# Performance work log

Measured on AMD Instinct MI355X. Metric: run time of the kernel, lower is better.

Reference implementation:

```python
import jax, jax.numpy as jnp
import numpy as np

EPS_MSG = 1e-7   # GENConv message epsilon
BN_EPS = 1e-5    # BatchNorm1d eps
NUM_GRAPHS = 1024


def _linear(x, W, b):
    return x @ W + b


def _batchnorm(x, gamma, beta):
    # training-mode batch statistics over the node dimension
    mu = jnp.mean(x, axis=0)
    var = jnp.mean((x - mu) ** 2, axis=0)
    return (x - mu) * jax.lax.rsqrt(var + BN_EPS) * gamma + beta


def _genconv(x, src, dst, e, t, W1, b1, gamma, beta, W2, b2, num_nodes):
    # message: relu(x_j + edge_attr) + eps, shape [E, H]
    msg = jax.nn.relu(x[src] + e) + EPS_MSG
    # learnable softmax aggregation over each destination's neighborhood
    s = msg * t
    m = jax.lax.stop_gradient(jax.ops.segment_max(s, dst, num_segments=num_nodes))
    m = jnp.where(jnp.isfinite(m), m, 0.0)
    ex = jnp.exp(s - m[dst])
    denom = jax.ops.segment_sum(ex, dst, num_segments=num_nodes)
    alpha = ex / (denom[dst] + 1e-16)
    agg = jax.ops.segment_sum(msg * alpha, dst, num_segments=num_nodes)  # [N, H]
    # GENConv MLP([H, 2H, H], norm='batch') applied to x + aggregated messages
    h = x + agg
    h = _linear(h, W1, b1)
    h = _batchnorm(h, gamma, beta)
    h = jax.nn.relu(h)
    return _linear(h, W2, b2)


def setup_inputs() -> dict:
    key = jax.random.key(0)
    N, E, FIN, FE, H, L, G, OUT = 50000, 1000000, 32, 16, 64, 4, NUM_GRAPHS, 1
    ks = jax.random.split(key, 32)

    def rn(k, shape, fan_in):
        return jax.random.normal(k, shape, dtype=jnp.float32) * (1.0 / np.sqrt(fan_in))

    inp = {}
    inp["x"] = jax.random.normal(ks[0], (N, FIN), dtype=jnp.float32)
    inp["edge_attr"] = jax.random.normal(ks[1], (E, FE), dtype=jnp.float32)
    inp["edge_index"] = jax.random.randint(ks[2], (2, E), 0, N)
    inp["batch"] = jnp.sort(jax.random.randint(ks[3], (N,), 0, G))
    # atom encoder: Linear(FIN,H) ReLU Linear(H,H) ReLU
    inp["atom_W1"] = rn(ks[4], (FIN, H), FIN); inp["atom_b1"] = jnp.zeros((H,), jnp.float32)
    inp["atom_W2"] = rn(ks[5], (H, H), H);     inp["atom_b2"] = jnp.zeros((H,), jnp.float32)
    # bond encoder: Linear(FE,H) ReLU Linear(H,H) ReLU
    inp["bond_W1"] = rn(ks[6], (FE, H), FE);   inp["bond_b1"] = jnp.zeros((H,), jnp.float32)
    inp["bond_W2"] = rn(ks[7], (H, H), H);     inp["bond_b2"] = jnp.zeros((H,), jnp.float32)
    # stacked GENConv params (L layers)
    inp["conv_t"] = jnp.ones((L,), jnp.float32)
    inp["conv_W1"] = rn(ks[8], (L, H, 2 * H), H)
    inp["conv_b1"] = jnp.zeros((L, 2 * H), jnp.float32)
    inp["conv_gamma"] = jnp.ones((L, 2 * H), jnp.float32)
    inp["conv_beta"] = jnp.zeros((L, 2 * H), jnp.float32)
    inp["conv_W2"] = rn(ks[9], (L, 2 * H, H), 2 * H)
    inp["conv_b2"] = jnp.zeros((L, H), jnp.float32)
    # head
    inp["lin1_W"] = rn(ks[10], (H, H), H);     inp["lin1_b"] = jnp.zeros((H,), jnp.float32)
    inp["lin2_W"] = rn(ks[11], (H, OUT), H);   inp["lin2_b"] = jnp.zeros((OUT,), jnp.float32)
    return inp


def reference(x, edge_attr, atom_W1, atom_b1, atom_W2, atom_b2,
              bond_W1, bond_b1, bond_W2, bond_b2,
              conv_t, conv_W1, conv_b1, conv_gamma, conv_beta, conv_W2, conv_b2,
              lin1_W, lin1_b, lin2_W, lin2_b,
              edge_index, batch):
    N = x.shape[0]
    src, dst = edge_index[0], edge_index[1]
    h = jax.nn.relu(_linear(jax.nn.relu(_linear(x, atom_W1, atom_b1)), atom_W2, atom_b2))
    e = jax.nn.relu(_linear(jax.nn.relu(_linear(edge_attr, bond_W1, bond_b1)), bond_W2, bond_b2))
    L = conv_t.shape[0]
    for i in range(L):
        h = _genconv(h, src, dst, e, conv_t[i], conv_W1[i], conv_b1[i],
                     conv_gamma[i], conv_beta[i], conv_W2[i], conv_b2[i], N)
        if i < L - 1:
            h = jax.nn.relu(h)
    g = jax.ops.segment_sum(h, batch, num_segments=NUM_GRAPHS)  # global_add_pool
    g = jax.nn.relu(_linear(g, lin1_W, lin1_b))
    return _linear(g, lin2_W, lin2_b)
```

## Files before the change

kernel.cpp:

```cpp
#include <hip/hip_runtime.h>
#include <hip/hip_bf16.h>
#include <math.h>

typedef __attribute__((ext_vector_type(8))) short bf16x8;
typedef __attribute__((ext_vector_type(4))) float f32x4;

__device__ inline unsigned f2bf(float f) {
    union { __hip_bfloat16 h; unsigned short u; } cv;
    cv.h = __float2bfloat16(f);
    return (unsigned)cv.u;
}


__global__ void k_hist(const int* __restrict__ dst, int* __restrict__ counts, int E) {
    int e = blockIdx.x * blockDim.x + threadIdx.x;
    if (e < E) atomicAdd(&counts[dst[e]], 1);
}

__global__ void k_scan1(const int* __restrict__ counts, int* __restrict__ row_ptr,
                        int* __restrict__ csum, int n) {
    __shared__ int buf[1024];
    int tid = threadIdx.x;
    int base = blockIdx.x * 1024;
    int v = (base + tid < n) ? counts[base + tid] : 0;
    buf[tid] = v;
    __syncthreads();
    int inc = v;
    for (int off = 1; off < 1024; off <<= 1) {
        int add = (tid >= off) ? buf[tid - off] : 0;
        __syncthreads();
        inc += add;
        buf[tid] = inc;
        __syncthreads();
    }
    if (base + tid < n) row_ptr[base + tid] = inc - v;
    if (tid == 1023) csum[blockIdx.x] = inc;
}

__global__ void k_scan2(int* __restrict__ csum, int nc, int* __restrict__ total) {
    if (threadIdx.x == 0) {
        int run = 0;
        for (int i = 0; i < nc; ++i) { int c = csum[i]; csum[i] = run; run += c; }
        *total = run;
    }
}

__global__ void k_scan3(int* __restrict__ row_ptr, const int* __restrict__ csum,
                        const int* __restrict__ total, int n) {
    int i = blockIdx.x * blockDim.x + threadIdx.x;
    if (i < n) row_ptr[i] += csum[i >> 10];
    if (i == 0) row_ptr[n] = *total;
}

#define ECH 4096
__global__ __launch_bounds__(256) void k_scatter(const int* __restrict__ src,
                          const int* __restrict__ dst,
                          const int* __restrict__ row_ptr, int* __restrict__ fill,
                          int2* __restrict__ spe, int E, int NS) {
    int bs = blockIdx.x & 7;
    int chunk = blockIdx.x >> 3;
    int base = chunk * ECH;
    int lo = bs * NS, hi = lo + NS;
#pragma unroll 1
    for (int j = 0; j < ECH / 256; ++j) {
        int e = base + j * 256 + threadIdx.x;
        if (e < E) {
            int d = dst[e];
            if (d >= lo && d < hi) {
                int pos = row_ptr[d] + atomicAdd(&fill[d], 1);
                spe[pos] = make_int2(src[e], e);
            }
        }
    }
}

__global__ void k_gptr(const int* __restrict__ batch, int* __restrict__ gptr, int n, int G) {
    int i = blockIdx.x * blockDim.x + threadIdx.x;
    if (i > n) return;
    if (i == 0) {
        int b0 = batch[0];
        for (int g = 0; g <= b0; ++g) gptr[g] = 0;
    } else if (i == n) {
        int bl = batch[n - 1];
        for (int g = bl + 1; g <= G; ++g) gptr[g] = n;
    } else {
        int b = batch[i], pb = batch[i - 1];
        for (int g = pb + 1; g <= b; ++g) gptr[g] = i;
    }
}


__global__ void k_wt(const float* __restrict__ W1, const float* __restrict__ W2,
                     float* __restrict__ W1t, unsigned short* __restrict__ W2tb) {
    int tid = blockIdx.x * blockDim.x + threadIdx.x;
    if (tid < 1024) {
        int j = tid / 16, k = tid % 16;
        W1t[j * 16 + k] = W1[k * 64 + j];
    }
    if (tid < 4096) {
        int j = tid / 64, k = tid % 64;
        W2tb[j * 64 + k] = (unsigned short)f2bf(W2[k * 64 + j]);
    }
}


#define TM 128
__global__ __launch_bounds__(256) void k_atom(const float* __restrict__ x,
        const float* __restrict__ W1, const float* __restrict__ b1,
        const float* __restrict__ W2, const float* __restrict__ b2,
        float* __restrict__ out, int M) {
    __shared__ float sU[TM * 65];
    __shared__ float sW1[32 * 64];
    __shared__ float sW2[64 * 64];
    __shared__ float sB1[64], sB2[64];
#define A_IN(r, c) sU[(r) * 33 + (c)]
#define A_T1(r, c) sU[(r) * 65 + (c)]
    int tid = threadIdx.x;
    int base = blockIdx.x * TM;
    for (int i = tid; i < 32 * 64 / 4; i += 256) ((float4*)sW1)[i] = ((const float4*)W1)[i];
    for (int i = tid; i < 64 * 64 / 4; i += 256) ((float4*)sW2)[i] = ((const float4*)W2)[i];
    if (tid < 64) { sB1[tid] = b1[tid]; sB2[tid] = b2[tid]; }
    for (int i = tid; i < TM * 32 / 4; i += 256) {
        int r = i / 8, c4 = i % 8;
        int row = base + r;
        float4 v = (row < M) ? ((const float4*)(x + (long)row * 32))[c4] : make_float4(0, 0, 0, 0);
        A_IN(r, c4 * 4 + 0) = v.x; A_IN(r, c4 * 4 + 1) = v.y;
        A_IN(r, c4 * 4 + 2) = v.z; A_IN(r, c4 * 4 + 3) = v.w;
    }
    __syncthreads();
    int r0 = (tid / 16) * 8;
    int c0 = (tid % 16) * 4;
    float acc[8][4];
#pragma unroll
    for (int i = 0; i < 8; i++)
#pragma unroll
        for (int j = 0; j < 4; j++) acc[i][j] = sB1[c0 + j];
    for (int k = 0; k < 32; k++) {
        float a[8], b[4];
#pragma unroll
        for (int i = 0; i < 8; i++) a[i] = A_IN(r0 + i, k);
#pragma unroll
        for (int j = 0; j < 4; j++) b[j] = sW1[k * 64 + c0 + j];
#pragma unroll
        for (int i = 0; i < 8; i++)
#pragma unroll
            for (int j = 0; j < 4; j++) acc[i][j] += a[i] * b[j];
    }
    __syncthreads();
#pragma unroll
    for (int i = 0; i < 8; i++)
#pragma unroll
        for (int j = 0; j < 4; j++) A_T1(r0 + i, c0 + j) = fmaxf(acc[i][j], 0.f);
    __syncthreads();
#pragma unroll
    for (int i = 0; i < 8; i++)
#pragma unroll
        for (int j = 0; j < 4; j++) acc[i][j] = sB2[c0 + j];
    for (int k = 0; k < 64; k++) {
        float a[8], b[4];
#pragma unroll
        for (int i = 0; i < 8; i++) a[i] = A_T1(r0 + i, k);
#pragma unroll
        for (int j = 0; j < 4; j++) b[j] = sW2[k * 64 + c0 + j];
#pragma unroll
        for (int i = 0; i < 8; i++)
#pragma unroll
            for (int j = 0; j < 4; j++) acc[i][j] += a[i] * b[j];
    }
#pragma unroll
    for (int i = 0; i < 8; i++) {
        int row = base + r0 + i;
        if (row < M) {
            float4 v = make_float4(fmaxf(acc[i][0], 0.f), fmaxf(acc[i][1], 0.f),
                                   fmaxf(acc[i][2], 0.f), fmaxf(acc[i][3], 0.f));
            *(float4*)(out + (long)row * 64 + c0) = v;
        }
    }
}


__global__ __launch_bounds__(256) void k_bond(const float* __restrict__ ea,
        const int2* __restrict__ spe,
        const float* __restrict__ W1t, const float* __restrict__ b1,
        const unsigned short* __restrict__ W2tb, const float* __restrict__ b2,
        __hip_bfloat16* __restrict__ e_out, int E) {
    __shared__ unsigned sT1[128 * 32];
    __shared__ unsigned sW2[64 * 32];
    int tid = threadIdx.x;

    for (int i = tid; i < 2048; i += 256) {
        int rw = i >> 5, cp = i & 31;
        sW2[rw * 32 + (cp ^ ((rw & 7) << 2))] = ((const unsigned*)W2tb)[i];
    }

    int ed = tid & 127;
    int h0 = __builtin_amdgcn_readfirstlane(tid >> 7);
    long gid = (long)blockIdx.x * 128 + ed;
    float in[16];
    if (gid < (long)E) {
        int src_e = spe[gid].y;
        const float4* er = (const float4*)(ea + (long)src_e * 16);
        float4 q0 = er[0], q1 = er[1], q2 = er[2], q3 = er[3];
        in[0] = q0.x; in[1] = q0.y; in[2] = q0.z; in[3] = q0.w;
        in[4] = q1.x; in[5] = q1.y; in[6] = q1.z; in[7] = q1.w;
        in[8] = q2.x; in[9] = q2.y; in[10] = q2.z; in[11] = q2.w;
        in[12] = q3.x; in[13] = q3.y; in[14] = q3.z; in[15] = q3.w;
    } else {
#pragma unroll
        for (int k = 0; k < 16; ++k) in[k] = 0.f;
    }

#pragma unroll
    for (int c = 0; c < 16; ++c) {
        float a0 = b1[h0 * 32 + 2 * c];
        float a1 = b1[h0 * 32 + 2 * c + 1];
#pragma unroll
        for (int k = 0; k < 16; ++k) {
            a0 = fmaf(in[k], W1t[(h0 * 32 + 2 * c) * 16 + k], a0);
            a1 = fmaf(in[k], W1t[(h0 * 32 + 2 * c + 1) * 16 + k], a1);
        }
        unsigned v = f2bf(fmaxf(a0, 0.f)) | (f2bf(fmaxf(a1, 0.f)) << 16);
        int cp = h0 * 16 + c;
        sT1[ed * 32 + (cp ^ ((ed & 7) << 2))] = v;
    }
    __syncthreads();

    int wv = tid >> 6, lane = tid & 63;
    int lr = lane & 15, q = lane >> 4;
    bf16x8 bf[4][2];
#pragma unroll
    for (int nt = 0; nt < 4; ++nt)
#pragma unroll
        for (int ks = 0; ks < 2; ++ks) {
            int rw = nt * 16 + lr;
            int u = rw * 32 + ((ks * 16 + q * 4) ^ ((rw & 7) << 2));
            bf[nt][ks] = *(const bf16x8*)&sW2[u];
        }
    f32x4 acc[2][4];
#pragma unroll
    for (int mt = 0; mt < 2; ++mt)
#pragma unroll
        for (int nt = 0; nt < 4; ++nt) {
            float bias = b2[nt * 16 + lr];
            f32x4 c0; c0[0] = bias; c0[1] = bias; c0[2] = bias; c0[3] = bias;
            acc[mt][nt] = c0;
        }
#pragma unroll
    for (int mt = 0; mt < 2; ++mt) {
        int rw = (wv * 2 + mt) * 16 + lr;
#pragma unroll
        for (int ks = 0; ks < 2; ++ks) {
            int u = rw * 32 + ((ks * 16 + q * 4) ^ ((rw & 7) << 2));
            bf16x8 af = *(const bf16x8*)&sT1[u];
#pragma unroll
            for (int nt = 0; nt < 4; ++nt)
                acc[mt][nt] = __builtin_amdgcn_mfma_f32_16x16x32_bf16(
                    af, bf[nt][ks], acc[mt][nt], 0, 0, 0);
        }
    }
    unsigned short* ob = (unsigned short*)e_out;
#pragma unroll
    for (int mt = 0; mt < 2; ++mt)
#pragma unroll
        for (int nt = 0; nt < 4; ++nt)
#pragma unroll
            for (int i = 0; i < 4; ++i) {
                long row = (long)blockIdx.x * 128 + (wv * 2 + mt) * 16 + q * 4 + i;
                if (row < (long)E)
                    ob[row * 64 + nt * 16 + lr] =
                        (unsigned short)f2bf(fmaxf(acc[mt][nt][i], 0.f));
            }
}


__global__ __launch_bounds__(256) void k_agg(const float* __restrict__ h,
        const __hip_bfloat16* __restrict__ eperm, const int2* __restrict__ spe,
        const int* __restrict__ row_ptr, const float* __restrict__ t_ptr, int layer,
        float* __restrict__ y, int n) {
    int wid = blockIdx.x * 4 + (threadIdx.x >> 6);
    int lane = threadIdx.x & 63;
    if (wid >= n) return;
    wid = __builtin_amdgcn_readfirstlane(wid);
    float tval = t_ptr[layer];
    int beg = row_ptr[wid], end = row_ptr[wid + 1];
    float m = -INFINITY, den = 0.f, num = 0.f;
    int i = beg;
    int rem = (end - beg) & 3;
    for (int r = 0; r < rem; ++r, ++i) {
        int s = spe[i].x;
        float ev = __bfloat162float(eperm[(long)i * 64 + lane]);
        float hv = h[(long)s * 64 + lane];
        float msg = fmaxf(hv + ev, 0.f) + 1e-7f;
        float sv = msg * tval;
        float mn = fmaxf(m, sv);
        float sc = __expf(m - mn);
        float w = __expf(sv - mn);
        den = den * sc + w;
        num = num * sc + w * msg;
        m = mn;
    }
    for (; i < end; i += 4) {
        int s0 = spe[i].x, s1 = spe[i + 1].x, s2 = spe[i + 2].x, s3 = spe[i + 3].x;
        float ev0 = __bfloat162float(eperm[(long)i * 64 + lane]);
        float ev1 = __bfloat162float(eperm[(long)(i + 1) * 64 + lane]);
        float ev2 = __bfloat162float(eperm[(long)(i + 2) * 64 + lane]);
        float ev3 = __bfloat162float(eperm[(long)(i + 3) * 64 + lane]);
        float hv0 = h[(long)s0 * 64 + lane];
        float hv1 = h[(long)s1 * 64 + lane];
        float hv2 = h[(long)s2 * 64 + lane];
        float hv3 = h[(long)s3 * 64 + lane];
        float msg0 = fmaxf(hv0 + ev0, 0.f) + 1e-7f;
        float msg1 = fmaxf(hv1 + ev1, 0.f) + 1e-7f;
        float msg2 = fmaxf(hv2 + ev2, 0.f) + 1e-7f;
        float msg3 = fmaxf(hv3 + ev3, 0.f) + 1e-7f;
        float sv0 = msg0 * tval, sv1 = msg1 * tval;
        float sv2 = msg2 * tval, sv3 = msg3 * tval;
        float mn = fmaxf(fmaxf(fmaxf(m, sv0), fmaxf(sv1, sv2)), sv3);
        float sc = __expf(m - mn);
        float w0 = __expf(sv0 - mn);
        float w1 = __expf(sv1 - mn);
        float w2 = __expf(sv2 - mn);
        float w3 = __expf(sv3 - mn);
        den = den * sc + ((w0 + w1) + (w2 + w3));
        num = num * sc + ((w0 * msg0 + w1 * msg1) + (w2 * msg2 + w3 * msg3));
        m = mn;
    }
    float agg = (end > beg) ? num / (den + 1e-16f) : 0.f;
    y[(long)wid * 64 + lane] = h[(long)wid * 64 + lane] + agg;
}


__global__ __launch_bounds__(256) void k_gemm1(const float* __restrict__ y,
        const float* __restrict__ W1, const float* __restrict__ b1,
        float* __restrict__ h1, float* __restrict__ part, int n) {
    __shared__ float sA[64][65];
    __shared__ float sW[64 * 128];
    __shared__ float sB[128];
    __shared__ float sS[8][128];
    __shared__ float sS2[8][128];
    int tid = threadIdx.x;
    int base = blockIdx.x * 64;
    for (int i = tid; i < 64 * 128 / 4; i += 256) ((float4*)sW)[i] = ((const float4*)W1)[i];
    if (tid < 128) sB[tid] = b1[tid];
    for (int i = tid; i < 64 * 64 / 4; i += 256) {
        int r = i / 16, c4 = i % 16;
        int row = base + r;
        float4 v = (row < n) ? ((const float4*)(y + (long)row * 64))[c4] : make_float4(0, 0, 0, 0);
        sA[r][c4 * 4 + 0] = v.x; sA[r][c4 * 4 + 1] = v.y;
        sA[r][c4 * 4 + 2] = v.z; sA[r][c4 * 4 + 3] = v.w;
    }
    __syncthreads();
    int rg = tid / 32;
    int r0 = rg * 8;
    int c0 = (tid % 32) * 4;
    float acc[8][4];
#pragma unroll
    for (int i = 0; i < 8; i++)
#pragma unroll
        for (int j = 0; j < 4; j++) acc[i][j] = sB[c0 + j];
    for (int k = 0; k < 64; k++) {
        float a[8], b[4];
#pragma unroll
        for (int i = 0; i < 8; i++) a[i] = sA[r0 + i][k];
#pragma unroll
        for (int j = 0; j < 4; j++) b[j] = sW[k * 128 + c0 + j];
#pragma unroll
        for (int i = 0; i < 8; i++)
#pragma unroll
            for (int j = 0; j < 4; j++) acc[i][j] += a[i] * b[j];
    }
    float ps[4] = {0, 0, 0, 0}, ps2[4] = {0, 0, 0, 0};
#pragma unroll
    for (int i = 0; i < 8; i++) {
        int row = base + r0 + i;
        if (row < n) {
            float4 v = make_float4(acc[i][0], acc[i][1], acc[i][2], acc[i][3]);
            *(float4*)(h1 + (long)row * 128 + c0) = v;
#pragma unroll
            for (int j = 0; j < 4; j++) { ps[j] += acc[i][j]; ps2[j] += acc[i][j] * acc[i][j]; }
        }
    }
#pragma unroll
    for (int j = 0; j < 4; j++) { sS[rg][c0 + j] = ps[j]; sS2[rg][c0 + j] = ps2[j]; }
    __syncthreads();
    if (tid < 128) {
        float s = 0.f, s2 = 0.f;
#pragma unroll
        for (int g = 0; g < 8; g++) { s += sS[g][tid]; s2 += sS2[g][tid]; }
        part[blockIdx.x * 256 + tid] = s;
        part[blockIdx.x * 256 + 128 + tid] = s2;
    }
}


__global__ __launch_bounds__(256) void k_bnred(const float* __restrict__ part,
                                               float* __restrict__ part2, int nblk) {
    int c = threadIdx.x;
    int b = blockIdx.x;
    float s = 0.f;
    for (int r = b; r < nblk; r += 64) s += part[r * 256 + c];
    part2[b * 256 + c] = s;
}

__global__ __launch_bounds__(1024) void k_bnfin(const float* __restrict__ part2,
                        const float* __restrict__ gamma, const float* __restrict__ beta,
                        float* __restrict__ scale, float* __restrict__ shift, float invN) {
    __shared__ float red[4][256];
    __shared__ float tot[256];
    int c = threadIdx.x & 255;
    int g = threadIdx.x >> 8;
    float s = 0.f;
#pragma unroll
    for (int r = 0; r < 16; ++r) s += part2[(g * 16 + r) * 256 + c];
    red[g][c] = s;
    __syncthreads();
    if (threadIdx.x < 256) tot[c] = red[0][c] + red[1][c] + red[2][c] + red[3][c];
    __syncthreads();
    if (threadIdx.x < 128) {
        int cc = threadIdx.x;
        float mu = tot[cc] * invN;
        float var = fmaxf(tot[128 + cc] * invN - mu * mu, 0.f);
        float sc = gamma[cc] * rsqrtf(var + 1e-5f);
        scale[cc] = sc;
        shift[cc] = beta[cc] - mu * sc;
    }
}


__global__ __launch_bounds__(256) void k_gemm2(const float* __restrict__ h1,
        const float* __restrict__ scale, const float* __restrict__ shift,
        const float* __restrict__ W2, const float* __restrict__ b2,
        float* __restrict__ hout, int n, int dorelu) {
    __shared__ float sA[32][129];
    __shared__ float sW[128 * 64];
    __shared__ float sSc[128], sSh[128], sB[64];
    int tid = threadIdx.x;
    int base = blockIdx.x * 32;
    for (int i = tid; i < 128 * 64 / 4; i += 256) ((float4*)sW)[i] = ((const float4*)W2)[i];
    if (tid < 128) { sSc[tid] = scale[tid]; sSh[tid] = shift[tid]; }
    if (tid < 64) sB[tid] = b2[tid];
    __syncthreads();
    for (int i = tid; i < 32 * 128 / 4; i += 256) {
        int r = i / 32, c4 = i % 32;
        int row = base + r;
        float4 v = (row < n) ? ((const float4*)(h1 + (long)row * 128))[c4] : make_float4(0, 0, 0, 0);
        int c = c4 * 4;
        sA[r][c + 0] = fmaxf(v.x * sSc[c + 0] + sSh[c + 0], 0.f);
        sA[r][c + 1] = fmaxf(v.y * sSc[c + 1] + sSh[c + 1], 0.f);
        sA[r][c + 2] = fmaxf(v.z * sSc[c + 2] + sSh[c + 2], 0.f);
        sA[r][c + 3] = fmaxf(v.w * sSc[c + 3] + sSh[c + 3], 0.f);
    }
    __syncthreads();
    int r0 = (tid / 16) * 2;
    int c0 = (tid % 16) * 4;
    float acc[2][4];
#pragma unroll
    for (int i = 0; i < 2; i++)
#pragma unroll
        for (int j = 0; j < 4; j++) acc[i][j] = sB[c0 + j];
    for (int k = 0; k < 128; k++) {
        float a[2], b[4];
#pragma unroll
        for (int i = 0; i < 2; i++) a[i] = sA[r0 + i][k];
#pragma unroll
        for (int j = 0; j < 4; j++) b[j] = sW[k * 64 + c0 + j];
#pragma unroll
        for (int i = 0; i < 2; i++)
#pragma unroll
            for (int j = 0; j < 4; j++) acc[i][j] += a[i] * b[j];
    }
#pragma unroll
    for (int i = 0; i < 2; i++) {
        int row = base + r0 + i;
        if (row < n) {
            float4 v;
            v.x = dorelu ? fmaxf(acc[i][0], 0.f) : acc[i][0];
            v.y = dorelu ? fmaxf(acc[i][1], 0.f) : acc[i][1];
            v.z = dorelu ? fmaxf(acc[i][2], 0.f) : acc[i][2];
            v.w = dorelu ? fmaxf(acc[i][3], 0.f) : acc[i][3];
            *(float4*)(hout + (long)row * 64 + c0) = v;
        }
    }
}


__global__ __launch_bounds__(64) void k_head(const float* __restrict__ h,
        const int* __restrict__ gptr,
        const float* __restrict__ W1, const float* __restrict__ b1,
        const float* __restrict__ W2, const float* __restrict__ b2,
        float* __restrict__ out) {
    int g = blockIdx.x;
    int lane = threadIdx.x;
    int beg = gptr[g], end = gptr[g + 1];
    float s = 0.f;
    for (int r = beg; r < end; ++r) s += h[(long)r * 64 + lane];
    __shared__ float sg[64];
    sg[lane] = s;
    __syncthreads();
    float acc = b1[lane];
    for (int k = 0; k < 64; k++) acc += sg[k] * W1[k * 64 + lane];
    acc = fmaxf(acc, 0.f);
    float v = acc * W2[lane];
#pragma unroll
    for (int off = 32; off > 0; off >>= 1) v += __shfl_down(v, off, 64);
    if (lane == 0) out[g] = v + b2[0];
}


extern "C" void kernel_launch(void* const* d_in, const int* in_sizes, int n_in,
                              void* d_out, int out_size, void* d_ws, size_t ws_size,
                              hipStream_t stream) {
    const float* x      = (const float*)d_in[0];
    const float* ea     = (const float*)d_in[1];
    const int*   ei     = (const int*)d_in[2];
    const int*   batch  = (const int*)d_in[3];
    const float* atomW1 = (const float*)d_in[4];
    const float* atomb1 = (const float*)d_in[5];
    const float* atomW2 = (const float*)d_in[6];
    const float* atomb2 = (const float*)d_in[7];
    const float* bondW1 = (const float*)d_in[8];
    const float* bondb1 = (const float*)d_in[9];
    const float* bondW2 = (const float*)d_in[10];
    const float* bondb2 = (const float*)d_in[11];
    const float* convT  = (const float*)d_in[12];
    const float* convW1 = (const float*)d_in[13];
    const float* convb1 = (const float*)d_in[14];
    const float* convG  = (const float*)d_in[15];
    const float* convBt = (const float*)d_in[16];
    const float* convW2 = (const float*)d_in[17];
    const float* convb2 = (const float*)d_in[18];
    const float* lin1W  = (const float*)d_in[19];
    const float* lin1b  = (const float*)d_in[20];
    const float* lin2W  = (const float*)d_in[21];
    const float* lin2b  = (const float*)d_in[22];
    float* out = (float*)d_out;

    const int N = in_sizes[0] / 32;
    const int E = in_sizes[1] / 16;
    const int G = out_size;
    const int Lconv = in_sizes[12];
    const int nchunk = (N + 1023) / 1024;
    const int nblk1 = (N + 63) / 64;
    const int NS = (N + 7) / 8;
    const int nchE = (E + ECH - 1) / ECH;

    size_t need = 0;
    auto count = [&](size_t bytes) { need += (bytes + 255) & ~(size_t)255; };
    count((size_t)E * 64 * 2);
    count((size_t)N * 64 * 4);
    count((size_t)N * 64 * 4);
    count((size_t)N * 128 * 4);
    count((size_t)E * 8);
    count((size_t)(N + 1) * 4);
    count((size_t)N * 4);
    count((size_t)N * 4);
    count((size_t)(G + 1) * 4);
    count((size_t)nblk1 * 256 * 4);
    count((size_t)64 * 256 * 4);
    count(128 * 4); count(128 * 4);
    count((size_t)(nchunk + 1) * 4);
    count(4);
    count(1024 * 4);
    count(4096 * 2);
    if (ws_size < need) {
        hipMemsetAsync(d_out, 0, (size_t)out_size * 4, stream);
        return;
    }

    char* ws = (char*)d_ws;
    size_t off = 0;
    auto alloc = [&](size_t bytes) -> void* {
        void* p = ws + off;
        off += (bytes + 255) & ~(size_t)255;
        return p;
    };
    __hip_bfloat16* e_perm = (__hip_bfloat16*)alloc((size_t)E * 64 * 2);
    float* h_cur    = (float*)alloc((size_t)N * 64 * 4);
    float* y_buf    = (float*)alloc((size_t)N * 64 * 4);
    float* h1       = (float*)alloc((size_t)N * 128 * 4);
    int2*  spe      = (int2*)alloc((size_t)E * 8);
    int*   row_ptr  = (int*)alloc((size_t)(N + 1) * 4);
    int*   counts   = (int*)alloc((size_t)N * 4);
    int*   fill     = (int*)alloc((size_t)N * 4);
    int*   gptr     = (int*)alloc((size_t)(G + 1) * 4);
    float* part     = (float*)alloc((size_t)nblk1 * 256 * 4);
    float* part2    = (float*)alloc((size_t)64 * 256 * 4);
    float* bnscale  = (float*)alloc(128 * 4);
    float* bnshift  = (float*)alloc(128 * 4);
    int*   csum     = (int*)alloc((size_t)(nchunk + 1) * 4);
    int*   totalp   = (int*)alloc(4);
    float* W1t      = (float*)alloc(1024 * 4);
    unsigned short* W2tb = (unsigned short*)alloc(4096 * 2);
    (void)n_in;

    hipMemsetAsync(counts, 0, (size_t)N * 4, stream);
    hipMemsetAsync(fill, 0, (size_t)N * 4, stream);

    const int* src = ei;
    const int* dst = ei + E;

    k_hist<<<(E + 255) / 256, 256, 0, stream>>>(dst, counts, E);
    k_scan1<<<nchunk, 1024, 0, stream>>>(counts, row_ptr, csum, N);
    k_scan2<<<1, 64, 0, stream>>>(csum, nchunk, totalp);
    k_scan3<<<(N + 255) / 256, 256, 0, stream>>>(row_ptr, csum, totalp, N);
    k_scatter<<<nchE * 8, 256, 0, stream>>>(src, dst, row_ptr, fill, spe, E, NS);
    k_gptr<<<(N + 256) / 256, 256, 0, stream>>>(batch, gptr, N, G);
    k_wt<<<16, 256, 0, stream>>>(bondW1, bondW2, W1t, W2tb);

    k_atom<<<(N + TM - 1) / TM, 256, 0, stream>>>(x, atomW1, atomb1, atomW2, atomb2, h_cur, N);
    k_bond<<<(E + 127) / 128, 256, 0, stream>>>(ea, spe, W1t, bondb1, W2tb, bondb2, e_perm, E);

    for (int l = 0; l < Lconv; ++l) {
        k_agg<<<(N + 3) / 4, 256, 0, stream>>>(h_cur, e_perm, spe, row_ptr, convT, l, y_buf, N);
        k_gemm1<<<nblk1, 256, 0, stream>>>(y_buf, convW1 + (size_t)l * 64 * 128,
                                           convb1 + (size_t)l * 128, h1, part, N);
        k_bnred<<<64, 256, 0, stream>>>(part, part2, nblk1);
        k_bnfin<<<1, 1024, 0, stream>>>(part2, convG + (size_t)l * 128, convBt + (size_t)l * 128,
                                        bnscale, bnshift, 1.0f / (float)N);
        k_gemm2<<<(N + 31) / 32, 256, 0, stream>>>(h1, bnscale, bnshift,
                                                   convW2 + (size_t)l * 128 * 64,
                                                   convb2 + (size_t)l * 64, h_cur, N,
                                                   (l < Lconv - 1) ? 1 : 0);
    }

    k_head<<<G, 64, 0, stream>>>(h_cur, gptr, lin1W, lin1b, lin2W, lin2b, out);
}
```

Baseline: 651.1 us.

## Interleave edge features in quads and use MFMA for bond first layer

The first bond-encoder linear layer now runs on bf16 MFMA instead of scalar FMAs, with the input edge attributes and W1 rounded to bf16. The CSR-ordered edge embedding buffer is stored in groups of four consecutive edges per feature lane, so the aggregation kernel loads four edge values with one 8-byte read instead of four 2-byte reads. The aggregation loop gains aligned head and tail handling to match the quad layout. This adds bf16 rounding of the raw edge inputs, which may slightly change accuracy.

```diff
diff --git a/kernel.cpp b/kernel.cpp
--- a/kernel.cpp
+++ b/kernel.cpp
@@ -9,6 +9,9 @@
     union { __hip_bfloat16 h; unsigned short u; } cv;
     cv.h = __float2bfloat16(f);
     return (unsigned)cv.u;
+}
+__device__ inline float bfu(unsigned u) {
+    return __uint_as_float(u << 16);
 }
 
 
@@ -91,11 +94,11 @@
 
 
 __global__ void k_wt(const float* __restrict__ W1, const float* __restrict__ W2,
-                     float* __restrict__ W1t, unsigned short* __restrict__ W2tb) {
+                     unsigned short* __restrict__ W1b, unsigned short* __restrict__ W2tb) {
     int tid = blockIdx.x * blockDim.x + threadIdx.x;
     if (tid < 1024) {
         int j = tid / 16, k = tid % 16;
-        W1t[j * 16 + k] = W1[k * 64 + j];
+        W1b[j * 16 + k] = (unsigned short)f2bf(W1[k * 64 + j]);
     }
     if (tid < 4096) {
         int j = tid / 64, k = tid % 64;
@@ -181,9 +184,9 @@
 
 __global__ __launch_bounds__(256) void k_bond(const float* __restrict__ ea,
         const int2* __restrict__ spe,
-        const float* __restrict__ W1t, const float* __restrict__ b1,
+        const unsigned short* __restrict__ W1b, const float* __restrict__ b1,
         const unsigned short* __restrict__ W2tb, const float* __restrict__ b2,
-        __hip_bfloat16* __restrict__ e_out, int E) {
+        unsigned short* __restrict__ e_q, int E) {
     __shared__ unsigned sT1[128 * 32];
     __shared__ unsigned sW2[64 * 32];
     int tid = threadIdx.x;
@@ -193,40 +196,54 @@
         sW2[rw * 32 + (cp ^ ((rw & 7) << 2))] = ((const unsigned*)W2tb)[i];
     }
 
-    int ed = tid & 127;
-    int h0 = __builtin_amdgcn_readfirstlane(tid >> 7);
-    long gid = (long)blockIdx.x * 128 + ed;
-    float in[16];
-    if (gid < (long)E) {
-        int src_e = spe[gid].y;
-        const float4* er = (const float4*)(ea + (long)src_e * 16);
-        float4 q0 = er[0], q1 = er[1], q2 = er[2], q3 = er[3];
-        in[0] = q0.x; in[1] = q0.y; in[2] = q0.z; in[3] = q0.w;
-        in[4] = q1.x; in[5] = q1.y; in[6] = q1.z; in[7] = q1.w;
-        in[8] = q2.x; in[9] = q2.y; in[10] = q2.z; in[11] = q2.w;
-        in[12] = q3.x; in[13] = q3.y; in[14] = q3.z; in[15] = q3.w;
-    } else {
-#pragma unroll
-        for (int k = 0; k < 16; ++k) in[k] = 0.f;
-    }
-
-#pragma unroll
-    for (int c = 0; c < 16; ++c) {
-        float a0 = b1[h0 * 32 + 2 * c];
-        float a1 = b1[h0 * 32 + 2 * c + 1];
-#pragma unroll
-        for (int k = 0; k < 16; ++k) {
-            a0 = fmaf(in[k], W1t[(h0 * 32 + 2 * c) * 16 + k], a0);
-            a1 = fmaf(in[k], W1t[(h0 * 32 + 2 * c + 1) * 16 + k], a1);
-        }
-        unsigned v = f2bf(fmaxf(a0, 0.f)) | (f2bf(fmaxf(a1, 0.f)) << 16);
-        int cp = h0 * 16 + c;
-        sT1[ed * 32 + (cp ^ ((ed & 7) << 2))] = v;
-    }
-    __syncthreads();
-
     int wv = tid >> 6, lane = tid & 63;
     int lr = lane & 15, q = lane >> 4;
+
+    union { bf16x8 v; uint4 u4; } bf1[4];
+    float bias1[4];
+#pragma unroll
+    for (int nt = 0; nt < 4; ++nt) {
+        bf1[nt].u4 = make_uint4(0, 0, 0, 0);
+        if (q < 2)
+            bf1[nt].u4 = *(const uint4*)(W1b + (nt * 16 + lr) * 16 + q * 8);
+        bias1[nt] = b1[nt * 16 + lr];
+    }
+
+#pragma unroll
+    for (int mt1 = 0; mt1 < 2; ++mt1) {
+        int rtile = wv * 2 + mt1;
+        long row1 = (long)blockIdx.x * 128 + rtile * 16 + lr;
+        long eidx = row1 < (long)E ? row1 : (long)(E - 1);
+        int eid = spe[eidx].y;
+        union { bf16x8 v; uint4 u4; unsigned u[4]; } af1;
+        af1.u4 = make_uint4(0, 0, 0, 0);
+        if (q < 2) {
+            const float4* er = (const float4*)(ea + (long)eid * 16 + q * 8);
+            float4 u0 = er[0], u1 = er[1];
+            af1.u[0] = f2bf(u0.x) | (f2bf(u0.y) << 16);
+            af1.u[1] = f2bf(u0.z) | (f2bf(u0.w) << 16);
+            af1.u[2] = f2bf(u1.x) | (f2bf(u1.y) << 16);
+            af1.u[3] = f2bf(u1.z) | (f2bf(u1.w) << 16);
+        }
+#pragma unroll
+        for (int nt = 0; nt < 4; ++nt) {
+            f32x4 c0;
+            c0[0] = bias1[nt]; c0[1] = bias1[nt]; c0[2] = bias1[nt]; c0[3] = bias1[nt];
+            f32x4 d = __builtin_amdgcn_mfma_f32_16x16x32_bf16(af1.v, bf1[nt].v, c0, 0, 0, 0);
+#pragma unroll
+            for (int i = 0; i < 4; ++i) {
+                unsigned hv = f2bf(fmaxf(d[i], 0.f));
+                unsigned ov = (unsigned)__shfl_xor((int)hv, 1, 64);
+                if ((lr & 1) == 0) {
+                    int r = rtile * 16 + q * 4 + i;
+                    int cp = nt * 8 + (lr >> 1);
+                    sT1[r * 32 + (cp ^ ((r & 7) << 2))] = hv | (ov << 16);
+                }
+            }
+        }
+    }
+    __syncthreads();
+
     bf16x8 bf[4][2];
 #pragma unroll
     for (int nt = 0; nt < 4; ++nt)
@@ -258,23 +275,30 @@
                     af, bf[nt][ks], acc[mt][nt], 0, 0, 0);
         }
     }
-    unsigned short* ob = (unsigned short*)e_out;
 #pragma unroll
     for (int mt = 0; mt < 2; ++mt)
 #pragma unroll
-        for (int nt = 0; nt < 4; ++nt)
-#pragma unroll
-            for (int i = 0; i < 4; ++i) {
-                long row = (long)blockIdx.x * 128 + (wv * 2 + mt) * 16 + q * 4 + i;
-                if (row < (long)E)
-                    ob[row * 64 + nt * 16 + lr] =
-                        (unsigned short)f2bf(fmaxf(acc[mt][nt][i], 0.f));
+        for (int nt = 0; nt < 4; ++nt) {
+            long r0 = (long)blockIdx.x * 128 + (wv * 2 + mt) * 16 + q * 4;
+            unsigned p01 = f2bf(fmaxf(acc[mt][nt][0], 0.f)) |
+                           (f2bf(fmaxf(acc[mt][nt][1], 0.f)) << 16);
+            unsigned p23 = f2bf(fmaxf(acc[mt][nt][2], 0.f)) |
+                           (f2bf(fmaxf(acc[mt][nt][3], 0.f)) << 16);
+            long qb = ((r0 >> 2) * 64 + nt * 16 + lr) * 4;
+            if (r0 + 3 < (long)E) {
+                *(uint2*)(e_q + qb) = make_uint2(p01, p23);
+            } else {
+                unsigned vv[4] = {p01 & 0xffff, p01 >> 16, p23 & 0xffff, p23 >> 16};
+#pragma unroll
+                for (int i = 0; i < 4; ++i)
+                    if (r0 + i < (long)E) e_q[qb + i] = (unsigned short)vv[i];
             }
+        }
 }
 
 
 __global__ __launch_bounds__(256) void k_agg(const float* __restrict__ h,
-        const __hip_bfloat16* __restrict__ eperm, const int2* __restrict__ spe,
+        const unsigned short* __restrict__ e_q, const int2* __restrict__ spe,
         const int* __restrict__ row_ptr, const float* __restrict__ t_ptr, int layer,
         float* __restrict__ y, int n) {
     int wid = blockIdx.x * 4 + (threadIdx.x >> 6);
@@ -285,10 +309,11 @@
     int beg = row_ptr[wid], end = row_ptr[wid + 1];
     float m = -INFINITY, den = 0.f, num = 0.f;
     int i = beg;
-    int rem = (end - beg) & 3;
-    for (int r = 0; r < rem; ++r, ++i) {
+    int astart = (beg + 3) & ~3; if (astart > end) astart = end;
+    int aend = end & ~3;         if (aend < astart) aend = astart;
+    for (; i < astart; ++i) {
         int s = spe[i].x;
-        float ev = __bfloat162float(eperm[(long)i * 64 + lane]);
+        float ev = bfu((unsigned)e_q[((long)(i >> 2) * 64 + lane) * 4 + (i & 3)]);
         float hv = h[(long)s * 64 + lane];
         float msg = fmaxf(hv + ev, 0.f) + 1e-7f;
         float sv = msg * tval;
@@ -299,12 +324,11 @@
         num = num * sc + w * msg;
         m = mn;
     }
-    for (; i < end; i += 4) {
+    for (; i < aend; i += 4) {
         int s0 = spe[i].x, s1 = spe[i + 1].x, s2 = spe[i + 2].x, s3 = spe[i + 3].x;
-        float ev0 = __bfloat162float(eperm[(long)i * 64 + lane]);
-        float ev1 = __bfloat162float(eperm[(long)(i + 1) * 64 + lane]);
-        float ev2 = __bfloat162float(eperm[(long)(i + 2) * 64 + lane]);
-        float ev3 = __bfloat162float(eperm[(long)(i + 3) * 64 + lane]);
+        uint2 ee = *(const uint2*)(e_q + ((long)(i >> 2) * 64 + lane) * 4);
+        float ev0 = bfu(ee.x & 0xffff), ev1 = bfu(ee.x >> 16);
+        float ev2 = bfu(ee.y & 0xffff), ev3 = bfu(ee.y >> 16);
         float hv0 = h[(long)s0 * 64 + lane];
         float hv1 = h[(long)s1 * 64 + lane];
         float hv2 = h[(long)s2 * 64 + lane];
@@ -323,6 +347,19 @@
         float w3 = __expf(sv3 - mn);
         den = den * sc + ((w0 + w1) + (w2 + w3));
         num = num * sc + ((w0 * msg0 + w1 * msg1) + (w2 * msg2 + w3 * msg3));
+        m = mn;
+    }
+    for (; i < end; ++i) {
+        int s = spe[i].x;
+        float ev = bfu((unsigned)e_q[((long)(i >> 2) * 64 + lane) * 4 + (i & 3)]);
+        float hv = h[(long)s * 64 + lane];
+        float msg = fmaxf(hv + ev, 0.f) + 1e-7f;
+        float sv = msg * tval;
+        float mn = fmaxf(m, sv);
+        float sc = __expf(m - mn);
+        float w = __expf(sv - mn);
+        den = den * sc + w;
+        num = num * sc + w * msg;
         m = mn;
     }
     float agg = (end > beg) ? num / (den + 1e-16f) : 0.f;
@@ -543,10 +580,11 @@
     const int nblk1 = (N + 63) / 64;
     const int NS = (N + 7) / 8;
     const int nchE = (E + ECH - 1) / ECH;
+    const size_t nquad = (size_t)((E + 3) / 4);
 
     size_t need = 0;
     auto count = [&](size_t bytes) { need += (bytes + 255) & ~(size_t)255; };
-    count((size_t)E * 64 * 2);
+    count(nquad * 4 * 64 * 2);
     count((size_t)N * 64 * 4);
     count((size_t)N * 64 * 4);
     count((size_t)N * 128 * 4);
@@ -560,7 +598,7 @@
     count(128 * 4); count(128 * 4);
     count((size_t)(nchunk + 1) * 4);
     count(4);
-    count(1024 * 4);
+    count(1024 * 2);
     count(4096 * 2);
     if (ws_size < need) {
         hipMemsetAsync(d_out, 0, (size_t)out_size * 4, stream);
@@ -574,7 +612,7 @@
         off += (bytes + 255) & ~(size_t)255;
         return p;
     };
-    __hip_bfloat16* e_perm = (__hip_bfloat16*)alloc((size_t)E * 64 * 2);
+    unsigned short* e_q = (unsigned short*)alloc(nquad * 4 * 64 * 2);
     float* h_cur    = (float*)alloc((size_t)N * 64 * 4);
     float* y_buf    = (float*)alloc((size_t)N * 64 * 4);
     float* h1       = (float*)alloc((size_t)N * 128 * 4);
@@ -589,7 +627,7 @@
     float* bnshift  = (float*)alloc(128 * 4);
     int*   csum     = (int*)alloc((size_t)(nchunk + 1) * 4);
     int*   totalp   = (int*)alloc(4);
-    float* W1t      = (float*)alloc(1024 * 4);
+    unsigned short* W1b  = (unsigned short*)alloc(1024 * 2);
     unsigned short* W2tb = (unsigned short*)alloc(4096 * 2);
     (void)n_in;
 
@@ -605,13 +643,13 @@
     k_scan3<<<(N + 255) / 256, 256, 0, stream>>>(row_ptr, csum, totalp, N);
     k_scatter<<<nchE * 8, 256, 0, stream>>>(src, dst, row_ptr, fill, spe, E, NS);
     k_gptr<<<(N + 256) / 256, 256, 0, stream>>>(batch, gptr, N, G);
-    k_wt<<<16, 256, 0, stream>>>(bondW1, bondW2, W1t, W2tb);
+    k_wt<<<16, 256, 0, stream>>>(bondW1, bondW2, W1b, W2tb);
 
     k_atom<<<(N + TM - 1) / TM, 256, 0, stream>>>(x, atomW1, atomb1, atomW2, atomb2, h_cur, N);
-    k_bond<<<(E + 127) / 128, 256, 0, stream>>>(ea, spe, W1t, bondb1, W2tb, bondb2, e_perm, E);
+    k_bond<<<(E + 127) / 128, 256, 0, stream>>>(ea, spe, W1b, bondb1, W2tb, bondb2, e_q, E);
 
     for (int l = 0; l < Lconv; ++l) {
-        k_agg<<<(N + 3) / 4, 256, 0, stream>>>(h_cur, e_perm, spe, row_ptr, convT, l, y_buf, N);
+        k_agg<<<(N + 3) / 4, 256, 0, stream>>>(h_cur, e_q, spe, row_ptr, convT, l, y_buf, N);
         k_gemm1<<<nblk1, 256, 0, stream>>>(y_buf, convW1 + (size_t)l * 64 * 128,
                                            convb1 + (size_t)l * 128, h1, part, N);
         k_bnred<<<64, 256, 0, stream>>>(part, part2, nblk1);
```

Result: no change. 656.5 us (+0.8%).
